# Performance work log

Hardware: AMD Instinct MI355X
Metric: run time of the kernel (lower is better)

## Reference

```python
import jax, jax.numpy as jnp
import numpy as np

S, B, C = 7, 2, 20
L_COORD, L_NOOBJ = 5.0, 0.5
BATCH = 16384


def setup_inputs() -> dict:
    key = jax.random.key(0)
    k1, k2, k3 = jax.random.split(key, 3)
    pred = jax.random.normal(k1, (BATCH, S, S, 5 * B + C), dtype=jnp.float32)
    target = jax.random.uniform(k2, (BATCH, S, S, 5 * B + C), dtype=jnp.float32)
    conf = target[..., 4]
    target = target.at[..., 4].set(jnp.where(conf > 0.9, conf, 0.0))
    # per-cell branch choice (replaces python random.random() > 0.5 per object)
    choice = jax.random.randint(k3, (BATCH, S, S), 0, 2, dtype=jnp.int32)
    return {"pred": pred, "target": target, "choice": choice}


def reference(pred, target, choice):
    dt = pred.dtype
    tconf = target[..., 4]
    obj = tconf > 0                      # [B,S,S]
    m = obj.astype(dt)
    n_obj = jnp.maximum(m.sum(), 1.0)
    c = choice.astype(bool)              # True -> box 1, False -> box 2
    cE = c[..., None]

    pxy = jnp.where(cE, pred[..., 0:2], pred[..., 5:7])
    pwh = jnp.where(cE, pred[..., 2:4], pred[..., 7:9])
    txy = jnp.where(cE, target[..., 0:2], target[..., 5:7])
    twh = jnp.where(cE, target[..., 2:4], target[..., 7:9])
    twh = jnp.where(obj[..., None], twh, 1.0)  # sqrt-safe outside obj mask
    pobj = jnp.where(c, pred[..., 4], pred[..., 9])
    tobj = jnp.where(c, tconf, target[..., 9])

    # per-object: mean over 2 elems for xy and for (wh - sqrt(twh)), summed over objects
    loc_cell = ((pxy - txy) ** 2).mean(-1) + ((pwh - jnp.sqrt(twh)) ** 2).mean(-1)
    loc_loss = L_COORD * (m * loc_cell).sum()
    obj_loss = (m * (pobj - tobj) ** 2).sum()

    nm = (tconf == 0).astype(dt)
    n_no = jnp.maximum(nm.sum(), 1.0)
    noobj_loss = L_NOOBJ * (
        (nm * (pred[..., 4] - tconf) ** 2).sum() / n_no
        + (nm * (pred[..., 9] - target[..., 9]) ** 2).sum() / n_no
    )

    # faithful to original: softmax applied BEFORE CrossEntropyLoss (double softmax)
    logits = pred[..., 5 * B:5 * B + C]
    sm = jax.nn.softmax(logits, axis=-1)
    logp = jax.nn.log_softmax(sm, axis=-1)
    tcls = jnp.argmax(target[..., 5 * B:5 * B + C], axis=-1)
    ce = -jnp.take_along_axis(logp, tcls[..., None], axis=-1)[..., 0]
    cls_loss = (m * ce).sum() / n_obj

    return (loc_loss, cls_loss, obj_loss, noobj_loss)
```

## Files before the change

kernel.cpp:

```cpp
#include <hip/hip_runtime.h>
#include <math.h>


constexpr int NCH = 30;
constexpr int CC  = 20;
constexpr int ROW = 8;
constexpr int T   = 128;
constexpr int CPB = 128;
constexpr int GRID = 1280;

__global__ __launch_bounds__(T) void yolo_main(
    const float* __restrict__ pred, const float* __restrict__ target,
    const int* __restrict__ choice, float* __restrict__ ws,
    int ncells, int nchunks)
{
    const int tid = threadIdx.x;

    float a_loc = 0.f, a_ce = 0.f, a_obj = 0.f, a_no = 0.f;
    float a_nob = 0.f, a_nno = 0.f;

    for (long long c = blockIdx.x; c < nchunks; c += GRID) {
        long long cell = c * CPB + tid;
        if (cell < (long long)ncells) {
            const float* sp  = pred   + cell * NCH;
            const float* stt = target + cell * NCH;
            float p[NCH], t[NCH];
            #pragma unroll
            for (int i = 0; i < NCH / 2; ++i) {
                float2 v = *(const float2*)&sp[2 * i];  p[2*i] = v.x; p[2*i+1] = v.y;
            }
            #pragma unroll
            for (int i = 0; i < NCH / 2; ++i) {
                float2 w = *(const float2*)&stt[2 * i]; t[2*i] = w.x; t[2*i+1] = w.y;
            }
            int myc = choice[cell];
            bool csel = myc != 0;

            float tconf = t[4];
            bool  obj = tconf > 0.0f;
            float m = obj ? 1.0f : 0.0f;

            float pxy0 = csel ? p[0] : p[5];
            float pxy1 = csel ? p[1] : p[6];
            float pwh0 = csel ? p[2] : p[7];
            float pwh1 = csel ? p[3] : p[8];
            float pobj = csel ? p[4] : p[9];
            float txy0 = csel ? t[0] : t[5];
            float txy1 = csel ? t[1] : t[6];
            float twh0 = csel ? t[2] : t[7];
            float twh1 = csel ? t[3] : t[8];
            if (!obj) { twh0 = 1.0f; twh1 = 1.0f; }
            float tobj = csel ? tconf : t[9];

            float dx = pxy0 - txy0, dy = pxy1 - txy1;
            float dw = pwh0 - sqrtf(twh0), dh = pwh1 - sqrtf(twh1);
            a_loc += m * (0.5f * (dx*dx + dy*dy) + 0.5f * (dw*dw + dh*dh));

            float dob = pobj - tobj;
            a_obj += m * dob * dob;

            float nm = (tconf == 0.0f) ? 1.0f : 0.0f;
            float d4 = p[4] - tconf, d9 = p[9] - t[9];
            a_no += nm * (d4 * d4 + d9 * d9);

            a_nob += m;
            a_nno += nm;

            int   tcls  = 0;
            float tbest = t[10];
            #pragma unroll
            for (int i = 1; i < CC; ++i) {
                float v = t[10 + i];
                if (v > tbest) { tbest = v; tcls = i; }
            }
            float mx = p[10];
            #pragma unroll
            for (int i = 1; i < CC; ++i) mx = fmaxf(mx, p[10 + i]);
            float e[CC];
            float Z = 0.f;
            #pragma unroll
            for (int i = 0; i < CC; ++i) { e[i] = __expf(p[10+i] - mx); Z += e[i]; }
            float rZ = 1.0f / Z;
            float Z2 = 0.f, sm_t = 0.f;
            #pragma unroll
            for (int i = 0; i < CC; ++i) {
                float sm = e[i] * rZ;
                Z2 += __expf(sm);
                if (i == tcls) sm_t = sm;
            }
            a_ce += m * (__logf(Z2) - sm_t);
        }
    }

    #pragma unroll
    for (int off = 32; off > 0; off >>= 1) {
        a_loc += __shfl_down(a_loc, off);
        a_ce  += __shfl_down(a_ce,  off);
        a_obj += __shfl_down(a_obj, off);
        a_no  += __shfl_down(a_no,  off);
        a_nob += __shfl_down(a_nob, off);
        a_nno += __shfl_down(a_nno, off);
    }

    __shared__ float red[4][6];
    int wave = tid >> 6;
    int lane = tid & 63;
    if (tid < 6) { red[2][tid] = 0.f; red[3][tid] = 0.f; }
    if (lane == 0) {
        red[wave][0] = a_loc; red[wave][1] = a_ce;  red[wave][2] = a_obj;
        red[wave][3] = a_no;  red[wave][4] = a_nob; red[wave][5] = a_nno;
    }
    __syncthreads();
    if (tid < 6) {
        float v = red[0][tid] + red[1][tid] + red[2][tid] + red[3][tid];
        ws[(size_t)blockIdx.x * ROW + tid] = v;
    }
}

__global__ __launch_bounds__(256) void yolo_reduce(
    const float* __restrict__ ws, float* __restrict__ out, int nb)
{
    float s[6] = {0.f, 0.f, 0.f, 0.f, 0.f, 0.f};
    for (int b = threadIdx.x; b < nb; b += 256) {
        #pragma unroll
        for (int j = 0; j < 6; ++j) s[j] += ws[(size_t)b * ROW + j];
    }
    #pragma unroll
    for (int off = 32; off > 0; off >>= 1) {
        #pragma unroll
        for (int j = 0; j < 6; ++j) s[j] += __shfl_down(s[j], off);
    }
    __shared__ float red[4][6];
    int wave = threadIdx.x >> 6;
    int lane = threadIdx.x & 63;
    if (lane == 0) {
        #pragma unroll
        for (int j = 0; j < 6; ++j) red[wave][j] = s[j];
    }
    __syncthreads();
    if (threadIdx.x == 0) {
        float t[6];
        #pragma unroll
        for (int j = 0; j < 6; ++j)
            t[j] = red[0][j] + red[1][j] + red[2][j] + red[3][j];
        out[0] = 5.0f * t[0];
        out[1] = t[1] / fmaxf(t[4], 1.0f);
        out[2] = t[2];
        out[3] = 0.5f * t[3] / fmaxf(t[5], 1.0f);
    }
}

extern "C" void kernel_launch(void* const* d_in, const int* in_sizes, int n_in,
                              void* d_out, int out_size, void* d_ws, size_t ws_size,
                              hipStream_t stream) {
    const float* pred   = (const float*)d_in[0];
    const float* target = (const float*)d_in[1];
    const int*   choice = (const int*)d_in[2];
    float* out = (float*)d_out;
    float* ws  = (float*)d_ws;

    int ncells  = in_sizes[2];
    int nchunks = (ncells + CPB - 1) / CPB;
    int grid    = GRID < nchunks ? GRID : nchunks;
    yolo_main<<<grid, T, 0, stream>>>(pred, target, choice, ws, ncells, nchunks);
    yolo_reduce<<<1, 256, 0, stream>>>(ws, out, grid);
}
```

Measured before the change: 216.6 us.

## Software-pipeline cell loads with double-buffered register sets in grid-stride loop

Restructures the grid-stride loop so each thread prefetches the next chunk's pred/target/choice into a second register set before computing the current one. Scheduling barriers stop the compiler from sinking the loads, so memory latency overlaps with the softmax/loss math. Launch bounds now request 2 blocks per CU. The cost is roughly double the register footprint for cell data, which may lower occupancy or cause spills. With 16384×49 cells over 1280 blocks each block runs about 5 iterations, so there is some room for overlap.

```diff
diff --git a/kernel.cpp b/kernel.cpp
--- a/kernel.cpp
+++ b/kernel.cpp
@@ -9,7 +9,97 @@
 constexpr int CPB = 128;
 constexpr int GRID = 1280;
 
-__global__ __launch_bounds__(T) void yolo_main(
+struct CellRegs {
+    float p[NCH];
+    float t[NCH];
+    int   c;
+};
+
+__device__ __forceinline__ void load_cell(
+    const float* __restrict__ pred, const float* __restrict__ target,
+    const int* __restrict__ choice, long long cell, long long ncells,
+    CellRegs& R)
+{
+    long long cl = cell < ncells ? cell : ncells - 1;
+    const float* sp  = pred   + cl * NCH;
+    const float* stt = target + cl * NCH;
+    #pragma unroll
+    for (int i = 0; i < NCH / 2; ++i) {
+        float2 v = *(const float2*)&sp[2 * i];
+        R.p[2*i] = v.x; R.p[2*i+1] = v.y;
+    }
+    #pragma unroll
+    for (int i = 0; i < NCH / 2; ++i) {
+        float2 w = *(const float2*)&stt[2 * i];
+        R.t[2*i] = w.x; R.t[2*i+1] = w.y;
+    }
+    R.c = choice[cl];
+}
+
+__device__ __forceinline__ void accum_cell(
+    const CellRegs& R, float& a_loc, float& a_ce, float& a_obj,
+    float& a_no, float& a_nob, float& a_nno)
+{
+    const float* p = R.p;
+    const float* t = R.t;
+    bool csel = R.c != 0;
+
+    float tconf = t[4];
+    bool  obj = tconf > 0.0f;
+    float m = obj ? 1.0f : 0.0f;
+
+    float pxy0 = csel ? p[0] : p[5];
+    float pxy1 = csel ? p[1] : p[6];
+    float pwh0 = csel ? p[2] : p[7];
+    float pwh1 = csel ? p[3] : p[8];
+    float pobj = csel ? p[4] : p[9];
+    float txy0 = csel ? t[0] : t[5];
+    float txy1 = csel ? t[1] : t[6];
+    float twh0 = csel ? t[2] : t[7];
+    float twh1 = csel ? t[3] : t[8];
+    if (!obj) { twh0 = 1.0f; twh1 = 1.0f; }
+    float tobj = csel ? tconf : t[9];
+
+    float dx = pxy0 - txy0, dy = pxy1 - txy1;
+    float dw = pwh0 - sqrtf(twh0), dh = pwh1 - sqrtf(twh1);
+    a_loc += m * (0.5f * (dx*dx + dy*dy) + 0.5f * (dw*dw + dh*dh));
+
+    float dob = pobj - tobj;
+    a_obj += m * dob * dob;
+
+    float nm = (tconf == 0.0f) ? 1.0f : 0.0f;
+    float d4 = p[4] - tconf, d9 = p[9] - t[9];
+    a_no += nm * (d4 * d4 + d9 * d9);
+
+    a_nob += m;
+    a_nno += nm;
+
+    int   tcls  = 0;
+    float tbest = t[10];
+    #pragma unroll
+    for (int i = 1; i < CC; ++i) {
+        float v = t[10 + i];
+        if (v > tbest) { tbest = v; tcls = i; }
+    }
+    float mx = p[10];
+    #pragma unroll
+    for (int i = 1; i < CC; ++i) mx = fmaxf(mx, p[10 + i]);
+    float e[CC];
+    float Z = 0.f;
+    #pragma unroll
+    for (int i = 0; i < CC; ++i) { e[i] = __expf(p[10+i] - mx); Z += e[i]; }
+    float rZ = 1.0f / Z;
+    float Z2 = 0.f, sm_t = 0.f;
+    #pragma unroll
+    for (int i = 0; i < CC; ++i) {
+        float sm = e[i] * rZ;
+        Z2 += __expf(sm);
+        if (i == tcls) sm_t = sm;
+    }
+    a_ce += m * (__logf(Z2) - sm_t);
+}
+
+__global__ __launch_bounds__(T, 2) void yolo_main(
     const float* __restrict__ pred, const float* __restrict__ target,
     const int* __restrict__ choice, float* __restrict__ ws,
     int ncells, int nchunks)
@@ -19,77 +109,28 @@
     float a_loc = 0.f, a_ce = 0.f, a_obj = 0.f, a_no = 0.f;
     float a_nob = 0.f, a_nno = 0.f;
 
-    for (long long c = blockIdx.x; c < nchunks; c += GRID) {
-        long long cell = c * CPB + tid;
-        if (cell < (long long)ncells) {
-            const float* sp  = pred   + cell * NCH;
-            const float* stt = target + cell * NCH;
-            float p[NCH], t[NCH];
-            #pragma unroll
-            for (int i = 0; i < NCH / 2; ++i) {
-                float2 v = *(const float2*)&sp[2 * i];  p[2*i] = v.x; p[2*i+1] = v.y;
-            }
-            #pragma unroll
-            for (int i = 0; i < NCH / 2; ++i) {
-                float2 w = *(const float2*)&stt[2 * i]; t[2*i] = w.x; t[2*i+1] = w.y;
-            }
-            int myc = choice[cell];
-            bool csel = myc != 0;
-
-            float tconf = t[4];
-            bool  obj = tconf > 0.0f;
-            float m = obj ? 1.0f : 0.0f;
-
-            float pxy0 = csel ? p[0] : p[5];
-            float pxy1 = csel ? p[1] : p[6];
-            float pwh0 = csel ? p[2] : p[7];
-            float pwh1 = csel ? p[3] : p[8];
-            float pobj = csel ? p[4] : p[9];
-            float txy0 = csel ? t[0] : t[5];
-            float txy1 = csel ? t[1] : t[6];
-            float twh0 = csel ? t[2] : t[7];
-            float twh1 = csel ? t[3] : t[8];
-            if (!obj) { twh0 = 1.0f; twh1 = 1.0f; }
-            float tobj = csel ? tconf : t[9];
-
-            float dx = pxy0 - txy0, dy = pxy1 - txy1;
-            float dw = pwh0 - sqrtf(twh0), dh = pwh1 - sqrtf(twh1);
-            a_loc += m * (0.5f * (dx*dx + dy*dy) + 0.5f * (dw*dw + dh*dh));
-
-            float dob = pobj - tobj;
-            a_obj += m * dob * dob;
-
-            float nm = (tconf == 0.0f) ? 1.0f : 0.0f;
-            float d4 = p[4] - tconf, d9 = p[9] - t[9];
-            a_no += nm * (d4 * d4 + d9 * d9);
-
-            a_nob += m;
-            a_nno += nm;
-
-            int   tcls  = 0;
-            float tbest = t[10];
-            #pragma unroll
-            for (int i = 1; i < CC; ++i) {
-                float v = t[10 + i];
-                if (v > tbest) { tbest = v; tcls = i; }
-            }
-            float mx = p[10];
-            #pragma unroll
-            for (int i = 1; i < CC; ++i) mx = fmaxf(mx, p[10 + i]);
-            float e[CC];
-            float Z = 0.f;
-            #pragma unroll
-            for (int i = 0; i < CC; ++i) { e[i] = __expf(p[10+i] - mx); Z += e[i]; }
-            float rZ = 1.0f / Z;
-            float Z2 = 0.f, sm_t = 0.f;
-            #pragma unroll
-            for (int i = 0; i < CC; ++i) {
-                float sm = e[i] * rZ;
-                Z2 += __expf(sm);
-                if (i == tcls) sm_t = sm;
-            }
-            a_ce += m * (__logf(Z2) - sm_t);
-        }
+    CellRegs A, B;
+    long long c = blockIdx.x;
+    bool any = c < nchunks;
+    if (any) load_cell(pred, target, choice, c * CPB + tid, ncells, A);
+
+    while (any) {
+        long long c1 = c + GRID;
+        bool h1 = c1 < nchunks;
+        if (h1) load_cell(pred, target, choice, c1 * CPB + tid, ncells, B);
+        __builtin_amdgcn_sched_barrier(0);
+        if (c * CPB + tid < (long long)ncells)
+            accum_cell(A, a_loc, a_ce, a_obj, a_no, a_nob, a_nno);
+        if (!h1) break;
+
+        long long c2 = c1 + GRID;
+        bool h2 = c2 < nchunks;
+        if (h2) load_cell(pred, target, choice, c2 * CPB + tid, ncells, A);
+        __builtin_amdgcn_sched_barrier(0);
+        if (c1 * CPB + tid < (long long)ncells)
+            accum_cell(B, a_loc, a_ce, a_obj, a_no, a_nob, a_nno);
+        if (!h2) break;
+        c = c2;
     }
 
     #pragma unroll
```

Result: no change. 215.1 us (-0.7%).

## Stage cell data through LDS with coalesced vector loads and register prefetch

Applied to the files above, without the earlier changes.

Each wave now loads its 64 cells of pred and target as contiguous 16-byte nontemporal vector loads into registers, writes them to a per-wave LDS buffer, and reads per-cell rows from LDS. The next chunk's loads are issued before the current chunk is computed, giving software double buffering. This replaces the strided per-thread float2 global loads with fully coalesced loads and overlaps memory latency with compute. It costs about 31 KB of LDS per block and extra registers, which may reduce occupancy.

```diff
diff --git a/kernel.cpp b/kernel.cpp
--- a/kernel.cpp
+++ b/kernel.cpp
@@ -1,6 +1,8 @@
 #include <hip/hip_runtime.h>
 #include <math.h>
 
+
+typedef float vf4 __attribute__((ext_vector_type(4)));
 
 constexpr int NCH = 30;
 constexpr int CC  = 20;
@@ -9,21 +11,64 @@
 constexpr int CPB = 128;
 constexpr int GRID = 1280;
 
+constexpr int WFLOATS = 64 * NCH * 2;
+constexpr int WSTRIDE = 3968;
+
+__device__ __forceinline__ void stage_issue(
+    const float* __restrict__ pred, const float* __restrict__ target,
+    const int* __restrict__ choice, long long cc, long long ncells,
+    int w, int l, vf4 (&st)[15], int& ci)
+{
+    long long cell0 = cc * CPB + w * 64;
+    long long b30   = cell0 * NCH;
+    long long lim   = ncells * (long long)NCH - 4;
+    #pragma unroll
+    for (int s = 0; s < 15; ++s) {
+        int f = s * 256 + l * 4;
+        long long g = b30 + (f < 1920 ? f : f - 1920);
+        if (g > lim) g = lim;
+        const float* src = (f < 1920) ? (pred + g) : (target + g);
+        st[s] = __builtin_nontemporal_load((const vf4*)src);
+    }
+    long long ce = cell0 + l;
+    ci = (ce < ncells) ? __builtin_nontemporal_load(&choice[ce]) : 0;
+}
+
 __global__ __launch_bounds__(T) void yolo_main(
     const float* __restrict__ pred, const float* __restrict__ target,
     const int* __restrict__ choice, float* __restrict__ ws,
     int ncells, int nchunks)
 {
+    __shared__ __align__(16) float sl[2 * WSTRIDE];
     const int tid = threadIdx.x;
+    const int w = tid >> 6, l = tid & 63;
+    float* wb = &sl[w * WSTRIDE];
 
     float a_loc = 0.f, a_ce = 0.f, a_obj = 0.f, a_no = 0.f;
     float a_nob = 0.f, a_nno = 0.f;
 
-    for (long long c = blockIdx.x; c < nchunks; c += GRID) {
-        long long cell = c * CPB + tid;
+    vf4 st[15];
+    int ci_n = 0;
+    long long c = blockIdx.x;
+    bool any = c < (long long)nchunks;
+    if (any) stage_issue(pred, target, choice, c, ncells, w, l, st, ci_n);
+
+    long long ccur = c;
+    while (any) {
+        #pragma unroll
+        for (int s = 0; s < 15; ++s)
+            *(vf4*)&wb[s * 256 + l * 4] = st[s];
+        int myc = ci_n;
+
+        long long cn = ccur + GRID;
+        bool hn = cn < (long long)nchunks;
+        if (hn) stage_issue(pred, target, choice, cn, ncells, w, l, st, ci_n);
+        __builtin_amdgcn_sched_barrier(0);
+
+        long long cell = ccur * CPB + tid;
         if (cell < (long long)ncells) {
-            const float* sp  = pred   + cell * NCH;
-            const float* stt = target + cell * NCH;
+            const float* sp  = &wb[l * NCH];
+            const float* stt = &wb[1920 + l * NCH];
             float p[NCH], t[NCH];
             #pragma unroll
             for (int i = 0; i < NCH / 2; ++i) {
@@ -31,9 +76,8 @@
             }
             #pragma unroll
             for (int i = 0; i < NCH / 2; ++i) {
-                float2 w = *(const float2*)&stt[2 * i]; t[2*i] = w.x; t[2*i+1] = w.y;
-            }
-            int myc = choice[cell];
+                float2 u = *(const float2*)&stt[2 * i]; t[2*i] = u.x; t[2*i+1] = u.y;
+            }
             bool csel = myc != 0;
 
             float tconf = t[4];
@@ -90,6 +134,9 @@
             }
             a_ce += m * (__logf(Z2) - sm_t);
         }
+
+        if (!hn) break;
+        ccur = cn;
     }
 
     #pragma unroll
@@ -103,12 +150,11 @@
     }
 
     __shared__ float red[4][6];
-    int wave = tid >> 6;
     int lane = tid & 63;
     if (tid < 6) { red[2][tid] = 0.f; red[3][tid] = 0.f; }
     if (lane == 0) {
-        red[wave][0] = a_loc; red[wave][1] = a_ce;  red[wave][2] = a_obj;
-        red[wave][3] = a_no;  red[wave][4] = a_nob; red[wave][5] = a_nno;
+        red[w][0] = a_loc; red[w][1] = a_ce;  red[w][2] = a_obj;
+        red[w][3] = a_no;  red[w][4] = a_nob; red[w][5] = a_nno;
     }
     __syncthreads();
     if (tid < 6) {
```

Measured after the change: 196.8 us. 1.1x faster.
